# Performance work log

Hardware: AMD Instinct MI355X
Metric: run time of the kernel (lower is better)

The kernel has to match this reference:

```python
import jax, jax.numpy as jnp
import numpy as np
import math

BATCH, SEQ, HIDDEN, HEADS = 2, 2048, 1024, 16
HEAD_SIZE = HIDDEN // HEADS
NEG_INF = -10000.0  # faithful to the torch module's masking constant


def setup_inputs() -> dict:
    key = jax.random.key(0)
    k1, k2, k3, k4 = jax.random.split(key, 4)
    x = jax.random.normal(k1, (BATCH, SEQ, HIDDEN), dtype=jnp.float32)
    pos_table = jax.random.normal(k2, (SEQ, HIDDEN), dtype=jnp.float32) * 0.02
    # torch nn.Linear weight layout: [out_features, in_features]
    Wqkv = jax.random.normal(k3, (3 * HIDDEN, HIDDEN), dtype=jnp.float32) * (1.0 / math.sqrt(HIDDEN))
    Wout = jax.random.normal(k4, (HIDDEN, HIDDEN), dtype=jnp.float32) * (1.0 / math.sqrt(HIDDEN))
    return {"x": x, "pos_table": pos_table, "Wqkv": Wqkv, "Wout": Wout}


def reference(x, pos_table, Wqkv, Wout):
    b, n, h = x.shape
    # positional embedding added for Q/K projection only (V uses raw x)
    xp = x + pos_table[None, :n, :]
    qk = jnp.einsum('bnd,ed->bne', xp, Wqkv[: 2 * HIDDEN])          # [b, n, 2h]
    q, k = jnp.split(qk, 2, axis=-1)
    v = jnp.einsum('bnd,ed->bne', x, Wqkv[2 * HIDDEN:])             # [b, n, h]

    def to_heads(t):  # b n (h l) -> b h n l
        return t.reshape(b, n, HEADS, HEAD_SIZE).transpose(0, 2, 1, 3)

    q, k, v = to_heads(q), to_heads(k), to_heads(v)

    scores = jnp.einsum('bhql,bhkl->bhqk', q, k) / math.sqrt(HEAD_SIZE)
    q_ind = jnp.arange(n)[:, None]
    k_ind = jnp.arange(n)[None, :]
    mask = q_ind < k_ind                                            # True where future
    scores = jnp.where(mask, NEG_INF, scores)
    probs = jax.nn.softmax(scores, axis=-1)
    combined_v = jnp.einsum('bhqk,bhkl->bhql', probs, v)            # [b, h, n, l]
    combined_v = combined_v.transpose(0, 2, 1, 3).reshape(b, n, h)  # b h q l -> b q (h l)
    out = jnp.einsum('bnd,ed->bne', combined_v, Wout)
    return out
```

## Files before the change

kernel.cpp:

```cpp
#include <hip/hip_runtime.h>
#include <hip/hip_bf16.h>
#include <stdint.h>

#define BATCH 2
#define SEQ   2048
#define HID   1024
#define NHEAD 16
#define HD    64
#define MROWS (BATCH*SEQ)

typedef __attribute__((ext_vector_type(8))) short bf16x8;
typedef __attribute__((ext_vector_type(4))) float f32x4;

__device__ inline unsigned pk2(float a, float b){
  __hip_bfloat162 h = __float22bfloat162_rn(make_float2(a, b));
  union { __hip_bfloat162 h; unsigned u; } v; v.h = h;
  return v.u;
}
__device__ inline float fexp2(float x){
#if __has_builtin(__builtin_amdgcn_exp2f)
  return __builtin_amdgcn_exp2f(x);
#else
  return exp2f(x);
#endif
}
__device__ inline void lds_load16(const short* g, short* l){
  __builtin_amdgcn_global_load_lds(
      (const __attribute__((address_space(1))) void*)g,
      (__attribute__((address_space(3))) void*)l, 16, 0, 0);
}

__global__ __launch_bounds__(256) void cast_all(
    const float* __restrict__ x, const float* __restrict__ pos,
    const float* __restrict__ w1, const float* __restrict__ w2,
    short* __restrict__ xb, short* __restrict__ xv,
    short* __restrict__ o1, short* __restrict__ o2){
  int i = blockIdx.x * 256 + threadIdx.x;
  const int n0 = MROWS*HID/4;
  if (i < n0){
    float4 xa = ((const float4*)x)[i];
    float4 pa = ((const float4*)pos)[i & (SEQ*HID/4 - 1)];
    uint2 sb, sv;
    sb.x = pk2(xa.x + pa.x, xa.y + pa.y);
    sb.y = pk2(xa.z + pa.z, xa.w + pa.w);
    sv.x = pk2(xa.x, xa.y);
    sv.y = pk2(xa.z, xa.w);
    ((uint2*)xb)[i] = sb;
    ((uint2*)xv)[i] = sv;
  } else {
    int j = i - n0;
    const int n1 = 3*HID*HID/4;
    const float4* src; uint2* dst; int k;
    if (j < n1){ src = (const float4*)w1; dst = (uint2*)o1; k = j; }
    else       { src = (const float4*)w2; dst = (uint2*)o2; k = j - n1; }
    float4 a = src[k];
    uint2 s;
    s.x = pk2(a.x, a.y);
    s.y = pk2(a.z, a.w);
    dst[k] = s;
  }
}

template<bool F32OUT>
__global__ __launch_bounds__(256) void gemm_bt(
    const short* __restrict__ A0, const short* __restrict__ A1, int split_bx,
    const short* __restrict__ W, void* __restrict__ Cout, int K, int ldc,
    int gx, int qsb, float qscale){
  const int nwg  = gridDim.x;
  const int q    = nwg >> 3;
  const int wgid = (blockIdx.x % 8) * q + (blockIdx.x / 8);
  const int bx = wgid % gx, by = wgid / gx;

  __shared__ alignas(16) short As[2][128*32];
  __shared__ alignas(16) short Bs[2][128*32];
  const short* A = (bx < split_bx) ? A0 : A1;
  const int tid  = threadIdx.x;
  const int w    = tid >> 6, lane = tid & 63;
  const int g    = lane >> 4, c = lane & 15;
  const int wr   = w >> 1, wc = w & 1;

  f32x4 acc[4][4];
#pragma unroll
  for (int m = 0; m < 4; ++m)
#pragma unroll
    for (int n = 0; n < 4; ++n) acc[m][n] = (f32x4){0.f, 0.f, 0.f, 0.f};

  const short* Abase = A + (size_t)(by*128) * K;
  const short* Wbase = W + (size_t)(bx*128) * K;

  auto stage = [&](int buf, int kt){
#pragma unroll
    for (int j = 0; j < 2; ++j){
      int ci  = w*128 + j*64 + lane;
      int row = ci >> 2, sub = ci & 3;
      lds_load16(Abase + (size_t)row*K + kt + sub*8, &As[buf][(w*128 + j*64)*8]);
      lds_load16(Wbase + (size_t)row*K + kt + sub*8, &Bs[buf][(w*128 + j*64)*8]);
    }
  };

  const int nk = K >> 5;
  stage(0, 0);
  int buf = 0;
  for (int ki = 0; ki < nk; ++ki){
    __syncthreads();
    if (ki + 1 < nk) stage(buf ^ 1, (ki + 1) * 32);

    bf16x8 af[4], bfr[4];
#pragma unroll
    for (int m = 0; m < 4; ++m)
      af[m] = *(const bf16x8*)&As[buf][(wr*64 + m*16 + c)*32 + g*8];
#pragma unroll
    for (int n = 0; n < 4; ++n)
      bfr[n] = *(const bf16x8*)&Bs[buf][(wc*64 + n*16 + c)*32 + g*8];
    __builtin_amdgcn_s_setprio(1);
#pragma unroll
    for (int m = 0; m < 4; ++m)
#pragma unroll
      for (int n = 0; n < 4; ++n)
        acc[m][n] = __builtin_amdgcn_mfma_f32_16x16x32_bf16(af[m], bfr[n], acc[m][n], 0, 0, 0);
    __builtin_amdgcn_s_setprio(0);
    buf ^= 1;
  }

  const float sc = (bx < qsb) ? qscale : 1.0f;
  const int row0 = by*128 + wr*64;
  const int col0 = bx*128 + wc*64;
#pragma unroll
  for (int m = 0; m < 4; ++m)
#pragma unroll
    for (int n = 0; n < 4; ++n){
      size_t base = (size_t)(row0 + m*16 + g*4) * ldc + (col0 + n*16 + c);
      if constexpr (F32OUT){
#pragma unroll
        for (int r = 0; r < 4; ++r)
          ((float*)Cout)[base + (size_t)r*ldc] = acc[m][n][r] * sc;
      } else {
        short* p = (short*)Cout + base;
        unsigned u01 = pk2(acc[m][n][0]*sc, acc[m][n][1]*sc);
        unsigned u23 = pk2(acc[m][n][2]*sc, acc[m][n][3]*sc);
        p[0]             = (short)(u01 & 0xffff);
        p[(size_t)ldc]   = (short)(u01 >> 16);
        p[2*(size_t)ldc] = (short)(u23 & 0xffff);
        p[3*(size_t)ldc] = (short)(u23 >> 16);
      }
    }
}

__global__ __launch_bounds__(256) void attn_fwd(
    const short* __restrict__ qkv, short* __restrict__ out){
  const int bid = blockIdx.x;
  const int qt  = 31 - (bid >> 5);
  const int bh  = bid & 31;
  const int b   = bh >> 4, h = bh & 15;
  const int tid = threadIdx.x;
  const int w   = tid >> 6, lane = tid & 63;
  const int g   = lane >> 4, c = lane & 15;

  __shared__ alignas(16) short Ks[2][64*64];
  __shared__ alignas(16) short Vt[2][64*64];

  const int q0 = qt*64 + w*16;
  const size_t rowb = (size_t)b * SEQ;

  const short* qptr = qkv + (rowb + q0 + c)*3072 + h*HD;
  bf16x8 qf0 = *(const bf16x8*)(qptr + g*8);
  bf16x8 qf1 = *(const bf16x8*)(qptr + 32 + g*8);

  const short* kbase = qkv + rowb*3072 + HID   + h*HD;
  const short* vbase = qkv + rowb*3072 + 2*HID + h*HD;

  const int slot   = ((lane >> 5) << 5) | (((lane >> 2) & 3) << 3)
                   | (((lane >> 4) & 1) << 2) | (lane & 3);
  const int vchunk = slot >> 3, vcol = slot & 7;

  auto stageK = [&](int buf, int c0){
#pragma unroll
    for (int j = 0; j < 2; ++j){
      int pc  = w*128 + j*64 + lane;
      int row = pc >> 3;
      int lc  = (pc & 7) ^ (row & 7);
      lds_load16(kbase + (size_t)(c0 + row)*3072 + lc*8, &Ks[buf][(w*128 + j*64)*8]);
    }
  };
  auto loadV = [&](int c0, bf16x8& v0, bf16x8& v1){
    const short* vp = vbase + (size_t)(c0 + lane)*3072 + w*16;
    v0 = *(const bf16x8*)(vp);
    v1 = *(const bf16x8*)(vp + 8);
  };
  auto scatterV = [&](int buf, const bf16x8& v0, const bf16x8& v1){
#pragma unroll
    for (int j = 0; j < 8; ++j)
      Vt[buf][(w*16 + j)*64 + ((vchunk ^ (j & 7)) << 3) + vcol] = v0[j];
#pragma unroll
    for (int j = 0; j < 8; ++j)
      Vt[buf][(w*16 + 8 + j)*64 + ((vchunk ^ ((8 + j) & 7)) << 3) + vcol] = v1[j];
  };

  f32x4 ot[4];
#pragma unroll
  for (int dt = 0; dt < 4; ++dt) ot[dt] = (f32x4){0.f, 0.f, 0.f, 0.f};
  float mrow = -1e30f, lrow = 0.f;
  const int qg = q0 + c;

  {
    bf16x8 v0, v1;
    stageK(0, 0);
    loadV(0, v0, v1);
    scatterV(0, v0, v1);
  }
  int cur = 0;
  for (int ch = 0; ch <= qt; ++ch){
    const int c0 = ch * 64;
    __syncthreads();

    bf16x8 nv0, nv1;
    if (ch < qt){
      stageK(cur ^ 1, c0 + 64);
      loadV(c0 + 64, nv0, nv1);
    }

    f32x4 s[4];
    __builtin_amdgcn_s_setprio(1);
#pragma unroll
    for (int kt = 0; kt < 4; ++kt){
      int row = kt*16 + c;
      bf16x8 k0 = *(const bf16x8*)&Ks[cur][row*64 + ((g       ^ (row&7))<<3)];
      bf16x8 k1 = *(const bf16x8*)&Ks[cur][row*64 + (((4 + g) ^ (row&7))<<3)];
      f32x4 z = (f32x4){0.f, 0.f, 0.f, 0.f};
      s[kt] = __builtin_amdgcn_mfma_f32_16x16x32_bf16(k0, qf0, z, 0, 0, 0);
      s[kt] = __builtin_amdgcn_mfma_f32_16x16x32_bf16(k1, qf1, s[kt], 0, 0, 0);
    }
    __builtin_amdgcn_s_setprio(0);

    float pv[16];
#pragma unroll
    for (int kt = 0; kt < 4; ++kt)
#pragma unroll
      for (int r = 0; r < 4; ++r) pv[kt*4 + r] = s[kt][r];

    if (ch == qt){
#pragma unroll
      for (int kt = 0; kt < 4; ++kt)
#pragma unroll
        for (int r = 0; r < 4; ++r){
          int ki = c0 + kt*16 + g*4 + r;
          if (ki > qg) pv[kt*4 + r] = -1e30f;
        }
    }

    float a0 = fmaxf(fmaxf(pv[0],  pv[1]),  pv[2]);
    float a1 = fmaxf(fmaxf(pv[3],  pv[4]),  pv[5]);
    float a2 = fmaxf(fmaxf(pv[6],  pv[7]),  pv[8]);
    float a3 = fmaxf(fmaxf(pv[9],  pv[10]), pv[11]);
    float a4 = fmaxf(fmaxf(pv[12], pv[13]), pv[14]);
    float cm = fmaxf(fmaxf(fmaxf(a0, a1), a2), fmaxf(fmaxf(a3, a4), pv[15]));
    cm = fmaxf(cm, __shfl_xor(cm, 16));
    cm = fmaxf(cm, __shfl_xor(cm, 32));
    if (__any(cm > mrow + 8.0f)){
      float mnew  = fmaxf(mrow, cm);
      float alpha = fexp2(mrow - mnew);
      lrow *= alpha;
#pragma unroll
      for (int dt = 0; dt < 4; ++dt)
#pragma unroll
        for (int r = 0; r < 4; ++r) ot[dt][r] *= alpha;
      mrow = mnew;
    }
    float ps = 0.f;
#pragma unroll
    for (int i = 0; i < 16; ++i){ pv[i] = fexp2(pv[i] - mrow); ps += pv[i]; }
    ps += __shfl_xor(ps, 16);
    ps += __shfl_xor(ps, 32);
    lrow += ps;

    union { unsigned u[4]; bf16x8 v; } pb0, pb1;
    pb0.u[0] = pk2(pv[0],  pv[1]);  pb0.u[1] = pk2(pv[2],  pv[3]);
    pb0.u[2] = pk2(pv[4],  pv[5]);  pb0.u[3] = pk2(pv[6],  pv[7]);
    pb1.u[0] = pk2(pv[8],  pv[9]);  pb1.u[1] = pk2(pv[10], pv[11]);
    pb1.u[2] = pk2(pv[12], pv[13]); pb1.u[3] = pk2(pv[14], pv[15]);

    __builtin_amdgcn_s_setprio(1);
#pragma unroll
    for (int dt = 0; dt < 4; ++dt){
      int d = dt*16 + c;
      bf16x8 va0 = *(const bf16x8*)&Vt[cur][d*64 + ((g       ^ (d&7))<<3)];
      bf16x8 va1 = *(const bf16x8*)&Vt[cur][d*64 + (((4 + g) ^ (d&7))<<3)];
      ot[dt] = __builtin_amdgcn_mfma_f32_16x16x32_bf16(va0, pb0.v, ot[dt], 0, 0, 0);
      ot[dt] = __builtin_amdgcn_mfma_f32_16x16x32_bf16(va1, pb1.v, ot[dt], 0, 0, 0);
    }
    __builtin_amdgcn_s_setprio(0);

    if (ch < qt) scatterV(cur ^ 1, nv0, nv1);
    cur ^= 1;
  }

  float inv = 1.f / lrow;
  short* obase = out + (rowb + q0 + c)*HID + h*HD + g*4;
#pragma unroll
  for (int dt = 0; dt < 4; ++dt){
    uint2 uu;
    uu.x = pk2(ot[dt][0]*inv, ot[dt][1]*inv);
    uu.y = pk2(ot[dt][2]*inv, ot[dt][3]*inv);
    *(uint2*)(obase + dt*16) = uu;
  }
}

extern "C" void kernel_launch(void* const* d_in, const int* in_sizes, int n_in,
                              void* d_out, int out_size, void* d_ws, size_t ws_size,
                              hipStream_t stream){
  const float* x    = (const float*)d_in[0];
  const float* pos  = (const float*)d_in[1];
  const float* Wqkv = (const float*)d_in[2];
  const float* Wout = (const float*)d_in[3];

  short* xb     = (short*)d_ws;
  short* xv     = xb    + (size_t)MROWS*HID;
  short* wqkvb  = xv    + (size_t)MROWS*HID;
  short* woutb  = wqkvb + (size_t)3*HID*HID;
  short* qkv    = woutb + (size_t)HID*HID;
  short* attn_o = xb;

  cast_all<<<dim3(8192), 256, 0, stream>>>(x, pos, Wqkv, Wout,
                                           xb, xv, wqkvb, woutb);

  gemm_bt<false><<<dim3(768), 256, 0, stream>>>(xb, xv, 16, wqkvb, qkv, HID, 3*HID,
                                                24, 8, 0.18033688011112042f);

  attn_fwd<<<dim3(1024), 256, 0, stream>>>(qkv, attn_o);

  gemm_bt<true><<<dim3(256), 256, 0, stream>>>(attn_o, attn_o, 8, woutb, d_out, HID, HID,
                                               8, 0, 1.0f);
}
```

Measured before the change: 191.1 us.

## Widen attention blocks to 128 query rows with 8 waves sharing K/V tiles

Each attention workgroup now holds 8 waves covering 128 query rows instead of 4 waves covering 64, so each staged K/V chunk in shared memory is reused by twice as many waves. Global K/V loads per query drop, and the grid is halved to 512 blocks of 512 threads. Waves whose diagonal chunk comes earlier skip compute on the trailing chunk but still take part in staging and barriers, which adds some idle time and less even causal load balance.

```diff
diff --git a/kernel.cpp b/kernel.cpp
--- a/kernel.cpp
+++ b/kernel.cpp
@@ -146,10 +146,10 @@
     }
 }
 
-__global__ __launch_bounds__(256) void attn_fwd(
+__global__ __launch_bounds__(512) void attn_fwd(
     const short* __restrict__ qkv, short* __restrict__ out){
   const int bid = blockIdx.x;
-  const int qt  = 31 - (bid >> 5);
+  const int qt  = 15 - (bid >> 5);
   const int bh  = bid & 31;
   const int b   = bh >> 4, h = bh & 15;
   const int tid = threadIdx.x;
@@ -159,7 +159,7 @@
   __shared__ alignas(16) short Ks[2][64*64];
   __shared__ alignas(16) short Vt[2][64*64];
 
-  const int q0 = qt*64 + w*16;
+  const int q0 = qt*128 + w*16;
   const size_t rowb = (size_t)b * SEQ;
 
   const short* qptr = qkv + (rowb + q0 + c)*3072 + h*HD;
@@ -169,128 +169,127 @@
   const short* kbase = qkv + rowb*3072 + HID   + h*HD;
   const short* vbase = qkv + rowb*3072 + 2*HID + h*HD;
 
-  const int slot   = ((lane >> 5) << 5) | (((lane >> 2) & 3) << 3)
-                   | (((lane >> 4) & 1) << 2) | (lane & 3);
-  const int vchunk = slot >> 3, vcol = slot & 7;
+  const int vkv = lane;
+  const int vdb = w*8;
+  const int slot = ((vkv >> 5) << 5) | (((vkv >> 2) & 3) << 3)
+                 | (((vkv >> 4) & 1) << 2) | (vkv & 3);
+  const int schunk = slot >> 3, scol = slot & 7;
 
   auto stageK = [&](int buf, int c0){
-#pragma unroll
-    for (int j = 0; j < 2; ++j){
-      int pc  = w*128 + j*64 + lane;
-      int row = pc >> 3;
-      int lc  = (pc & 7) ^ (row & 7);
-      lds_load16(kbase + (size_t)(c0 + row)*3072 + lc*8, &Ks[buf][(w*128 + j*64)*8]);
-    }
+    int row = tid >> 3;
+    int lc  = (tid & 7) ^ (row & 7);
+    lds_load16(kbase + (size_t)(c0 + row)*3072 + lc*8, &Ks[buf][tid*8]);
   };
-  auto loadV = [&](int c0, bf16x8& v0, bf16x8& v1){
-    const short* vp = vbase + (size_t)(c0 + lane)*3072 + w*16;
-    v0 = *(const bf16x8*)(vp);
-    v1 = *(const bf16x8*)(vp + 8);
+  auto loadV = [&](int c0, bf16x8& v0){
+    v0 = *(const bf16x8*)(vbase + (size_t)(c0 + vkv)*3072 + vdb);
   };
-  auto scatterV = [&](int buf, const bf16x8& v0, const bf16x8& v1){
-#pragma unroll
-    for (int j = 0; j < 8; ++j)
-      Vt[buf][(w*16 + j)*64 + ((vchunk ^ (j & 7)) << 3) + vcol] = v0[j];
-#pragma unroll
-    for (int j = 0; j < 8; ++j)
-      Vt[buf][(w*16 + 8 + j)*64 + ((vchunk ^ ((8 + j) & 7)) << 3) + vcol] = v1[j];
+  auto scatterV = [&](int buf, const bf16x8& v0){
+#pragma unroll
+    for (int j = 0; j < 8; ++j){
+      int d = vdb + j;
+      Vt[buf][d*64 + ((schunk ^ (d & 7)) << 3) + scol] = v0[j];
+    }
   };
 
   f32x4 ot[4];
 #pragma unroll
   for (int dt = 0; dt < 4; ++dt) ot[dt] = (f32x4){0.f, 0.f, 0.f, 0.f};
   float mrow = -1e30f, lrow = 0.f;
-  const int qg = q0 + c;
+  const int qg  = q0 + c;
+  const int dch = q0 >> 6;
 
   {
-    bf16x8 v0, v1;
+    bf16x8 v0;
     stageK(0, 0);
-    loadV(0, v0, v1);
-    scatterV(0, v0, v1);
+    loadV(0, v0);
+    scatterV(0, v0);
   }
   int cur = 0;
-  for (int ch = 0; ch <= qt; ++ch){
+  const int nch = 2*qt + 2;
+  for (int ch = 0; ch < nch; ++ch){
     const int c0 = ch * 64;
     __syncthreads();
 
-    bf16x8 nv0, nv1;
-    if (ch < qt){
+    bf16x8 nv;
+    if (ch + 1 < nch){
       stageK(cur ^ 1, c0 + 64);
-      loadV(c0 + 64, nv0, nv1);
-    }
-
-    f32x4 s[4];
-    __builtin_amdgcn_s_setprio(1);
-#pragma unroll
-    for (int kt = 0; kt < 4; ++kt){
-      int row = kt*16 + c;
-      bf16x8 k0 = *(const bf16x8*)&Ks[cur][row*64 + ((g       ^ (row&7))<<3)];
-      bf16x8 k1 = *(const bf16x8*)&Ks[cur][row*64 + (((4 + g) ^ (row&7))<<3)];
-      f32x4 z = (f32x4){0.f, 0.f, 0.f, 0.f};
-      s[kt] = __builtin_amdgcn_mfma_f32_16x16x32_bf16(k0, qf0, z, 0, 0, 0);
-      s[kt] = __builtin_amdgcn_mfma_f32_16x16x32_bf16(k1, qf1, s[kt], 0, 0, 0);
-    }
-    __builtin_amdgcn_s_setprio(0);
-
-    float pv[16];
-#pragma unroll
-    for (int kt = 0; kt < 4; ++kt)
-#pragma unroll
-      for (int r = 0; r < 4; ++r) pv[kt*4 + r] = s[kt][r];
-
-    if (ch == qt){
+      loadV(c0 + 64, nv);
+    }
+
+    if (ch <= dch){
+      f32x4 s[4];
+      __builtin_amdgcn_s_setprio(1);
+#pragma unroll
+      for (int kt = 0; kt < 4; ++kt){
+        int row = kt*16 + c;
+        bf16x8 k0 = *(const bf16x8*)&Ks[cur][row*64 + ((g       ^ (row&7))<<3)];
+        bf16x8 k1 = *(const bf16x8*)&Ks[cur][row*64 + (((4 + g) ^ (row&7))<<3)];
+        f32x4 z = (f32x4){0.f, 0.f, 0.f, 0.f};
+        s[kt] = __builtin_amdgcn_mfma_f32_16x16x32_bf16(k0, qf0, z, 0, 0, 0);
+        s[kt] = __builtin_amdgcn_mfma_f32_16x16x32_bf16(k1, qf1, s[kt], 0, 0, 0);
+      }
+      __builtin_amdgcn_s_setprio(0);
+
+      float pv[16];
 #pragma unroll
       for (int kt = 0; kt < 4; ++kt)
 #pragma unroll
-        for (int r = 0; r < 4; ++r){
-          int ki = c0 + kt*16 + g*4 + r;
-          if (ki > qg) pv[kt*4 + r] = -1e30f;
-        }
-    }
-
-    float a0 = fmaxf(fmaxf(pv[0],  pv[1]),  pv[2]);
-    float a1 = fmaxf(fmaxf(pv[3],  pv[4]),  pv[5]);
-    float a2 = fmaxf(fmaxf(pv[6],  pv[7]),  pv[8]);
-    float a3 = fmaxf(fmaxf(pv[9],  pv[10]), pv[11]);
-    float a4 = fmaxf(fmaxf(pv[12], pv[13]), pv[14]);
-    float cm = fmaxf(fmaxf(fmaxf(a0, a1), a2), fmaxf(fmaxf(a3, a4), pv[15]));
-    cm = fmaxf(cm, __shfl_xor(cm, 16));
-    cm = fmaxf(cm, __shfl_xor(cm, 32));
-    if (__any(cm > mrow + 8.0f)){
-      float mnew  = fmaxf(mrow, cm);
-      float alpha = fexp2(mrow - mnew);
-      lrow *= alpha;
-#pragma unroll
-      for (int dt = 0; dt < 4; ++dt)
-#pragma unroll
-        for (int r = 0; r < 4; ++r) ot[dt][r] *= alpha;
-      mrow = mnew;
-    }
-    float ps = 0.f;
-#pragma unroll
-    for (int i = 0; i < 16; ++i){ pv[i] = fexp2(pv[i] - mrow); ps += pv[i]; }
-    ps += __shfl_xor(ps, 16);
-    ps += __shfl_xor(ps, 32);
-    lrow += ps;
-
-    union { unsigned u[4]; bf16x8 v; } pb0, pb1;
-    pb0.u[0] = pk2(pv[0],  pv[1]);  pb0.u[1] = pk2(pv[2],  pv[3]);
-    pb0.u[2] = pk2(pv[4],  pv[5]);  pb0.u[3] = pk2(pv[6],  pv[7]);
-    pb1.u[0] = pk2(pv[8],  pv[9]);  pb1.u[1] = pk2(pv[10], pv[11]);
-    pb1.u[2] = pk2(pv[12], pv[13]); pb1.u[3] = pk2(pv[14], pv[15]);
-
-    __builtin_amdgcn_s_setprio(1);
-#pragma unroll
-    for (int dt = 0; dt < 4; ++dt){
-      int d = dt*16 + c;
-      bf16x8 va0 = *(const bf16x8*)&Vt[cur][d*64 + ((g       ^ (d&7))<<3)];
-      bf16x8 va1 = *(const bf16x8*)&Vt[cur][d*64 + (((4 + g) ^ (d&7))<<3)];
-      ot[dt] = __builtin_amdgcn_mfma_f32_16x16x32_bf16(va0, pb0.v, ot[dt], 0, 0, 0);
-      ot[dt] = __builtin_amdgcn_mfma_f32_16x16x32_bf16(va1, pb1.v, ot[dt], 0, 0, 0);
-    }
-    __builtin_amdgcn_s_setprio(0);
-
-    if (ch < qt) scatterV(cur ^ 1, nv0, nv1);
+        for (int r = 0; r < 4; ++r) pv[kt*4 + r] = s[kt][r];
+
+      if (ch == dch){
+#pragma unroll
+        for (int kt = 0; kt < 4; ++kt)
+#pragma unroll
+          for (int r = 0; r < 4; ++r){
+            int ki = c0 + kt*16 + g*4 + r;
+            if (ki > qg) pv[kt*4 + r] = -1e30f;
+          }
+      }
+
+      float a0 = fmaxf(fmaxf(pv[0],  pv[1]),  pv[2]);
+      float a1 = fmaxf(fmaxf(pv[3],  pv[4]),  pv[5]);
+      float a2 = fmaxf(fmaxf(pv[6],  pv[7]),  pv[8]);
+      float a3 = fmaxf(fmaxf(pv[9],  pv[10]), pv[11]);
+      float a4 = fmaxf(fmaxf(pv[12], pv[13]), pv[14]);
+      float cm = fmaxf(fmaxf(fmaxf(a0, a1), a2), fmaxf(fmaxf(a3, a4), pv[15]));
+      cm = fmaxf(cm, __shfl_xor(cm, 16));
+      cm = fmaxf(cm, __shfl_xor(cm, 32));
+      if (__any(cm > mrow + 8.0f)){
+        float mnew  = fmaxf(mrow, cm);
+        float alpha = fexp2(mrow - mnew);
+        lrow *= alpha;
+#pragma unroll
+        for (int dt = 0; dt < 4; ++dt)
+#pragma unroll
+          for (int r = 0; r < 4; ++r) ot[dt][r] *= alpha;
+        mrow = mnew;
+      }
+      float ps = 0.f;
+#pragma unroll
+      for (int i = 0; i < 16; ++i){ pv[i] = fexp2(pv[i] - mrow); ps += pv[i]; }
+      ps += __shfl_xor(ps, 16);
+      ps += __shfl_xor(ps, 32);
+      lrow += ps;
+
+      union { unsigned u[4]; bf16x8 v; } pb0, pb1;
+      pb0.u[0] = pk2(pv[0],  pv[1]);  pb0.u[1] = pk2(pv[2],  pv[3]);
+      pb0.u[2] = pk2(pv[4],  pv[5]);  pb0.u[3] = pk2(pv[6],  pv[7]);
+      pb1.u[0] = pk2(pv[8],  pv[9]);  pb1.u[1] = pk2(pv[10], pv[11]);
+      pb1.u[2] = pk2(pv[12], pv[13]); pb1.u[3] = pk2(pv[14], pv[15]);
+
+      __builtin_amdgcn_s_setprio(1);
+#pragma unroll
+      for (int dt = 0; dt < 4; ++dt){
+        int d = dt*16 + c;
+        bf16x8 va0 = *(const bf16x8*)&Vt[cur][d*64 + ((g       ^ (d&7))<<3)];
+        bf16x8 va1 = *(const bf16x8*)&Vt[cur][d*64 + (((4 + g) ^ (d&7))<<3)];
+        ot[dt] = __builtin_amdgcn_mfma_f32_16x16x32_bf16(va0, pb0.v, ot[dt], 0, 0, 0);
+        ot[dt] = __builtin_amdgcn_mfma_f32_16x16x32_bf16(va1, pb1.v, ot[dt], 0, 0, 0);
+      }
+      __builtin_amdgcn_s_setprio(0);
+    }
+
+    if (ch + 1 < nch) scatterV(cur ^ 1, nv);
     cur ^= 1;
   }
 
@@ -326,7 +325,7 @@
   gemm_bt<false><<<dim3(768), 256, 0, stream>>>(xb, xv, 16, wqkvb, qkv, HID, 3*HID,
                                                 24, 8, 0.18033688011112042f);
 
-  attn_fwd<<<dim3(1024), 256, 0, stream>>>(qkv, attn_o);
+  attn_fwd<<<dim3(512), 512, 0, stream>>>(qkv, attn_o);
 
   gemm_bt<true><<<dim3(256), 256, 0, stream>>>(attn_o, attn_o, 8, woutb, d_out, HID, HID,
                                                8, 0, 1.0f);
```

Measured after the change: 195.9 us. +2.5%, slower.
